# Kernel optimization log

Hardware: AMD Instinct MI355X
Metric: run time of the kernel (lower is better)

The kernel has to match this reference:

```python
import jax, jax.numpy as jnp
import numpy as np

BN_EPS = 1e-5

def _bn(x, gamma, beta, relu=True):
    # training-mode BatchNorm over all dims except channel (last)
    axes = tuple(range(x.ndim - 1))
    mu = jnp.mean(x, axes, keepdims=True)
    var = jnp.var(x, axes, keepdims=True)
    y = (x - mu) / jnp.sqrt(var + BN_EPS) * gamma + beta
    return jax.nn.relu(y) if relu else y

def _l2norm(x, eps):
    # F.normalize: x / max(||x||, eps)
    n = jnp.sqrt(jnp.sum(x * x, axis=-1, keepdims=True))
    return x / jnp.maximum(n, eps)

def setup_inputs() -> dict:
    key = jax.random.key(0)
    ks = jax.random.split(key, 16)
    B, N, H, W, C = 2, 512, 16, 32, 64
    IN_DIM = 10 + C + C + 2  # 140
    MLP3 = [128, 64]
    s = 0.02
    inp = {
        "warped_xyz": jax.random.normal(ks[0], (B, N, 3), jnp.float32),
        "warped_points": jax.random.normal(ks[1], (B, N, C), jnp.float32),
        "RF3": jax.random.normal(ks[2], (B, C, H, W), jnp.float32),
        "RF3_index": jax.random.normal(ks[3], (B, 3, H, W), jnp.float32),
        "lidar_z": jax.random.uniform(ks[4], (B, N, 1), jnp.float32),
        # conv1x1 stack (mlp3)
        "W1": jax.random.normal(ks[5], (IN_DIM, MLP3[0]), jnp.float32) * s,
        "b1": jnp.zeros((MLP3[0],), jnp.float32),
        "g1": jnp.ones((MLP3[0],), jnp.float32),
        "be1": jnp.zeros((MLP3[0],), jnp.float32),
        "W2": jax.random.normal(ks[6], (MLP3[0], MLP3[1]), jnp.float32) * s,
        "b2": jnp.zeros((MLP3[1],), jnp.float32),
        "g2": jnp.ones((MLP3[1],), jnp.float32),
        "be2": jnp.zeros((MLP3[1],), jnp.float32),
        # conv1d stack (mlp4 = [feats_dim//2], then 2 logits)
        "M1w": jax.random.normal(ks[7], (MLP3[1], MLP3[1] // 2), jnp.float32) * s,
        "M1b": jnp.zeros((MLP3[1] // 2,), jnp.float32),
        "M1g": jnp.ones((MLP3[1] // 2,), jnp.float32),
        "M1be": jnp.zeros((MLP3[1] // 2,), jnp.float32),
        "M2w": jax.random.normal(ks[8], (MLP3[1] // 2, 2), jnp.float32) * s,
        "M2b": jnp.zeros((2,), jnp.float32),
    }
    return inp

def reference(warped_xyz, warped_points, RF3, RF3_index, lidar_z,
              W1, b1, g1, be1, W2, b2, g2, be2,
              M1w, M1b, M1g, M1be, M2w, M2b):
    B, N, _ = warped_xyz.shape
    _, Ci, H, W_ = RF3.shape
    M = H * W_
    RF3_bnc = RF3.transpose(0, 2, 3, 1).reshape(B, M, Ci)          # [B,M,C]
    idx_bnc = RF3_index.transpose(0, 2, 3, 1).reshape(B, M, 3)     # [B,M,3]

    src_xyz = warped_xyz[:, :, None, :]                             # [B,N,1,3]
    dst_xyz = idx_bnc[:, None, :, :]                                # [B,1,M,3]
    euc = (src_xyz - dst_xyz)[..., :2]                              # [B,N,M,2]
    euc_norm = jnp.sqrt(euc[..., 0:1] ** 2 + euc[..., 1:2] ** 2)    # [B,N,M,1]

    xyz_z = (warped_xyz * lidar_z)[:, :, None, :]                   # [B,N,1,3]
    src_pts = warped_points[:, :, None, :]                          # [B,N,1,C]
    dst_pts = RF3_bnc[:, None, :, :]                                # [B,1,M,C]

    geom = jnp.concatenate([
        jnp.broadcast_to(xyz_z, (B, N, M, 3)),
        jnp.broadcast_to(src_pts[..., :2], (B, N, M, 2)),
        jnp.broadcast_to(dst_xyz[..., :2], (B, N, M, 2)),
        euc, euc_norm], axis=-1)                                    # [B,N,M,10]
    desc = jnp.concatenate([
        jnp.broadcast_to(src_pts, (B, N, M, Ci)),
        jnp.broadcast_to(dst_pts, (B, N, M, Ci))], axis=-1)         # [B,N,M,2C]

    # cal_sim: cosine sim between lidar feats (src) and image feats (dst)
    src_n = _l2norm(warped_points, 1e-12)
    dst_n = _l2norm(RF3_bnc, 1e-12)
    cos = jnp.einsum('bnc,bmc->bnm', src_n, dst_n)                  # [B,N,M]
    s1 = cos / (jnp.max(cos, axis=2, keepdims=True) + 1e-6)         # src->dst norm
    s2 = cos / (jnp.max(cos, axis=1, keepdims=True) + 1e-10)        # dst->src norm
    sim = jnp.stack([s1, s2], axis=-1)                              # [B,N,M,2]

    feats = jnp.concatenate([geom, desc, sim], axis=-1)             # [B,N,M,140]
    feats = _bn(jnp.einsum('bnmi,io->bnmo', feats, W1) + b1, g1, be1)
    feats = _bn(jnp.einsum('bnmi,io->bnmo', feats, W2) + b2, g2, be2)

    aw = jax.nn.softmax(jnp.max(feats, axis=-1), axis=-1)           # [B,N,M]
    att = jnp.einsum('bnm,bnmc->bnc', aw, feats)                    # [B,N,C]

    att = _bn(att @ M1w + M1b, M1g, M1be)
    logits = att @ M2w + M2b                                        # [B,N,2]
    return logits
```

## Files before the change

kernel.cpp:

```cpp
#include <hip/hip_runtime.h>
#include <hip/hip_bf16.h>

#define B_ 2
#define N_ 512
#define M_ 512
#define C_ 64
#define O1 128
#define O2 64
#define O3 32
#define PBIG 524288.0f
#define P3   1024.0f

typedef short s8v __attribute__((ext_vector_type(8)));
typedef float f4v __attribute__((ext_vector_type(4)));

#define WS_SRCN 0
#define WS_DSTN 65536
#define WS_P0   0
#define WS_U    131072
#define WS_V    262144
#define WS_DXY  393216
#define WS_COS  395264
#define WS_RMAX 919552
#define WS_CMAX 920576
#define WS_ST1  921600
#define WS_ST2  925696
#define WS_ST3  927744
#define WS_Z    928768
#define WS_W2F  928768
#define WS_W9S  932864
#define WS_X2   961536

__device__ __forceinline__ unsigned fenc(float f){
  unsigned b = __float_as_uint(f);
  return (b & 0x80000000u) ? ~b : (b | 0x80000000u);
}
__device__ __forceinline__ float fdec(unsigned u){
  unsigned b = (u & 0x80000000u) ? (u & 0x7fffffffu) : ~u;
  return __uint_as_float(b);
}
__device__ __forceinline__ unsigned short f2bf(float f){
  unsigned u = __float_as_uint(f);
  unsigned r = (u + 0x7fffu + ((u >> 16) & 1u)) >> 16;
  return (unsigned short)r;
}
__device__ __forceinline__ float bf2f(unsigned short h){
  return __uint_as_float(((unsigned)h) << 16);
}
__device__ __forceinline__ unsigned pk_trunc(float lo, float hi){
  return __builtin_amdgcn_perm(__float_as_uint(hi), __float_as_uint(lo), 0x07060302u);
}
__device__ __forceinline__ f4v relu4(f4v z){
  z[0] = fmaxf(z[0], 0.f); z[1] = fmaxf(z[1], 0.f);
  z[2] = fmaxf(z[2], 0.f); z[3] = fmaxf(z[3], 0.f);
  return z;
}

__global__ __launch_bounds__(128) void k1a(const float* __restrict__ wxyz,
    const float* __restrict__ wpts, const float* __restrict__ lz,
    const float* __restrict__ W1, float* __restrict__ ws){
  int blk = blockIdx.x; int b = blk >> 9, n = blk & 511; int t = threadIdx.x;
  int bn = b*N_ + n;
  __shared__ float wp[64]; __shared__ float sxyz[3]; __shared__ float slz; __shared__ float srn;
  if (t < 64) wp[t] = wpts[bn*64 + t];
  if (t >= 64 && t < 67) sxyz[t-64] = wxyz[bn*3 + (t-64)];
  if (t == 67) slz = lz[bn];
  __syncthreads();
  if (t < 64){
    float v = wp[t]*wp[t];
    v += __shfl_down(v,32); v += __shfl_down(v,16); v += __shfl_down(v,8);
    v += __shfl_down(v,4);  v += __shfl_down(v,2);  v += __shfl_down(v,1);
    if (t == 0) srn = 1.0f / fmaxf(sqrtf(v), 1e-12f);
  }
  __syncthreads();
  if (t < 64) ws[WS_SRCN + bn*64 + t] = wp[t]*srn;
  int o = t;
  float x = sxyz[0], y = sxyz[1], z = sxyz[2], l = slz;
  float acc = x*l*W1[0*O1+o] + y*l*W1[1*O1+o] + z*l*W1[2*O1+o]
            + wp[0]*W1[3*O1+o] + wp[1]*W1[4*O1+o]
            + x*W1[7*O1+o] + y*W1[8*O1+o];
  #pragma unroll 8
  for (int c = 0; c < 64; ++c) acc += wp[c]*W1[(10+c)*O1+o];
  ws[WS_U + bn*O1 + o] = acc;
}

__global__ __launch_bounds__(128) void k1b(const float* __restrict__ rf3,
    const float* __restrict__ rf3i, const float* __restrict__ W1, float* __restrict__ ws){
  int blk = blockIdx.x; int b = blk >> 9, m = blk & 511; int t = threadIdx.x;
  int bm = b*M_ + m;
  __shared__ float rf[64]; __shared__ float sdx, sdy, srn;
  if (t < 64) rf[t] = rf3[(b*64 + t)*512 + m];
  if (t == 64) sdx = rf3i[(b*3 + 0)*512 + m];
  if (t == 65) sdy = rf3i[(b*3 + 1)*512 + m];
  __syncthreads();
  if (t < 64){
    float v = rf[t]*rf[t];
    v += __shfl_down(v,32); v += __shfl_down(v,16); v += __shfl_down(v,8);
    v += __shfl_down(v,4);  v += __shfl_down(v,2);  v += __shfl_down(v,1);
    if (t == 0) srn = 1.0f / fmaxf(sqrtf(v), 1e-12f);
  }
  __syncthreads();
  if (t < 64) ws[WS_DSTN + bm*64 + t] = rf[t]*srn;
  if (t == 0){ ws[WS_DXY + bm*2+0] = sdx; ws[WS_DXY + bm*2+1] = sdy; }
  int o = t;
  float acc = sdx*(W1[5*O1+o] - W1[7*O1+o]) + sdy*(W1[6*O1+o] - W1[8*O1+o]);
  #pragma unroll 8
  for (int c = 0; c < 64; ++c) acc += rf[c]*W1[(74+c)*O1+o];
  ws[WS_V + bm*O1 + o] = acc;
}

__global__ __launch_bounds__(256) void k2(float* __restrict__ ws){
  int blk = blockIdx.x; int b = blk >> 9, n = blk & 511; int t = threadIdx.x;
  int bn = b*N_ + n;
  __shared__ __align__(16) float sn[64];
  __shared__ float dnt[64*65];
  __shared__ float part[4*64];
  if (t < 64) sn[t] = ws[WS_SRCN + bn*64 + t];
  unsigned* cmax = (unsigned*)ws + WS_CMAX;
  float lmax = -1e30f;
  for (int chunk = 0; chunk < 8; ++chunk){
    __syncthreads();
    const float4* src = (const float4*)(ws + WS_DSTN + (size_t)(b*M_ + chunk*64)*64);
    #pragma unroll
    for (int i = 0; i < 4; ++i){
      float4 v = src[t + i*256];
      int base = (t + i*256)*4; int mm = base >> 6, c = base & 63;
      float* dp = &dnt[mm*65 + c];
      dp[0]=v.x; dp[1]=v.y; dp[2]=v.z; dp[3]=v.w;
    }
    __syncthreads();
    {
      int mm = t & 63, cg = t >> 6;
      const float* dr = &dnt[mm*65 + cg*16];
      const float* sr = &sn[cg*16];
      float p = 0.f;
      #pragma unroll
      for (int k = 0; k < 16; ++k) p += sr[k]*dr[k];
      part[cg*64 + mm] = p;
    }
    __syncthreads();
    if (t < 64){
      float d = part[t] + part[64+t] + part[128+t] + part[192+t];
      int m = chunk*64 + t;
      ws[WS_COS + bn*M_ + m] = d;
      atomicMax(&cmax[b*M_ + m], fenc(d));
      lmax = fmaxf(lmax, d);
    }
  }
  if (t < 64){
    lmax = fmaxf(lmax, __shfl_xor(lmax,32)); lmax = fmaxf(lmax, __shfl_xor(lmax,16));
    lmax = fmaxf(lmax, __shfl_xor(lmax,8));  lmax = fmaxf(lmax, __shfl_xor(lmax,4));
    lmax = fmaxf(lmax, __shfl_xor(lmax,2));  lmax = fmaxf(lmax, __shfl_xor(lmax,1));
    if (t == 0) ws[WS_RMAX + bn] = lmax;
  }
}

__global__ __launch_bounds__(256) void k3(const float* __restrict__ wxyz,
    const float* __restrict__ W1, const float* __restrict__ b1, float* __restrict__ ws){
  int blk = blockIdx.x; int b = blk >> 9, n = blk & 511; int t = threadIdx.x;
  int bn = b*N_ + n;
  __shared__ float s_en[512], s_s1[512], s_s2[512];
  __shared__ float sx, sy, srm;
  if (t == 0){ sx = wxyz[bn*3+0]; sy = wxyz[bn*3+1]; srm = ws[WS_RMAX+bn]; }
  __syncthreads();
  const unsigned* cmax = (const unsigned*)ws + WS_CMAX;
  #pragma unroll
  for (int i = 0; i < 2; ++i){
    int m = t + i*256;
    float dx = ws[WS_DXY + (b*M_+m)*2+0], dy = ws[WS_DXY + (b*M_+m)*2+1];
    float ex = sx-dx, ey = sy-dy;
    s_en[m] = sqrtf(ex*ex + ey*ey);
    float cv = ws[WS_COS + bn*M_ + m];
    s_s1[m] = cv/(srm + 1e-6f);
    s_s2[m] = cv/(fdec(cmax[b*M_+m]) + 1e-10f);
  }
  __syncthreads();
  int o = t & 127, mh = t >> 7;
  float u  = ws[WS_U + bn*O1 + o] + b1[o];
  float w9 = W1[9*O1+o], wa = W1[138*O1+o], wb = W1[139*O1+o];
  float sum = 0.f, ssq = 0.f;
  const float* Vp = ws + WS_V + b*M_*O1 + o;
  int mBeg = mh*256, mEnd = mBeg + 256;
  #pragma unroll 8
  for (int m = mBeg; m < mEnd; ++m){
    float xv = u + Vp[m*O1] + s_en[m]*w9 + s_s1[m]*wa + s_s2[m]*wb;
    sum += xv; ssq += xv*xv;
  }
  int rep = blk & 15;
  atomicAdd(&ws[WS_ST1 + rep*256 + o], sum);
  atomicAdd(&ws[WS_ST1 + rep*256 + 128 + o], ssq);
}

__global__ __launch_bounds__(128) void k3b(const float* __restrict__ W1,
    const float* __restrict__ b1, const float* __restrict__ g1,
    const float* __restrict__ be1, const float* __restrict__ W2, float* __restrict__ ws){
  int blk = blockIdx.x; int t = threadIdx.x;
  int o = t;
  float s = 0.f, q = 0.f;
  #pragma unroll
  for (int r = 0; r < 16; ++r){ s += ws[WS_ST1 + r*256 + o]; q += ws[WS_ST1 + r*256 + 128 + o]; }
  float mu = s/PBIG, var = q/PBIG - mu*mu;
  float istd = rsqrtf(var + 1e-5f);
  float A1 = g1[o]*istd, C1 = be1[o] - mu*A1;
  if (blk < 1024){
    int bn = blk;
    ws[WS_P0 + bn*O1 + o] = (ws[WS_U + bn*O1 + o] + b1[o])*A1 + C1;
  } else if (blk < 1040){
    int r0 = (blk - 1024)*64;
    for (int r = 0; r < 64; ++r)
      ws[WS_V + (size_t)(r0 + r)*O1 + o] *= A1;
  } else {
    ws[WS_W9S + o]       = W1[9*O1+o]*A1;
    ws[WS_W9S + 128 + o] = W1[138*O1+o]*A1;
    ws[WS_W9S + 256 + o] = W1[139*O1+o]*A1;
    unsigned short* wf = (unsigned short*)(ws + WS_W2F);
    for (int i = t; i < 8192; i += 128){
      int j = i & 7, ll = (i >> 3) & 63, ct = (i >> 9) & 3, k0q = i >> 11;
      int oo = k0q*32 + (ll >> 4)*8 + j, c = ct*16 + (ll & 15);
      wf[i] = f2bf(W2[oo*O2 + c]);
    }
  }
}

__global__ __launch_bounds__(256, 4) void k4(const float* __restrict__ wxyz,
    float* __restrict__ ws){
  int blk = blockIdx.x;
  int b = blk >> 11; int rem = blk & 2047; int n = rem >> 2; int mc = rem & 3;
  int t = threadIdx.x; int bn = b*N_ + n; int m0 = mc*128;
  __shared__ __align__(16) unsigned short wBf[8192];
  __shared__ __align__(16) float p0s[128], w9s[128], was[128], wbs[128];
  __shared__ float s_en[128], s_s1[128], s_s2[128];
  __shared__ float ls[64], lq[64];
  __shared__ float sx, sy, srm;
  if (t == 0){ sx = wxyz[bn*3+0]; sy = wxyz[bn*3+1]; srm = ws[WS_RMAX+bn]; }
  if (t < 64){ ls[t] = 0.f; lq[t] = 0.f; }
  {
    const s8v* g = (const s8v*)(ws + WS_W2F);
    s8v* l = (s8v*)wBf;
    #pragma unroll
    for (int c2 = 0; c2 < 4; ++c2) l[c2*256 + t] = g[c2*256 + t];
  }
  if (t < 128){
    p0s[t] = ws[WS_P0 + bn*O1 + t];
    w9s[t] = ws[WS_W9S + t];
    was[t] = ws[WS_W9S + 128 + t];
    wbs[t] = ws[WS_W9S + 256 + t];
  }
  __syncthreads();
  if (t < 128){
    int m = m0 + t;
    float dx = ws[WS_DXY + (b*M_+m)*2+0], dy = ws[WS_DXY + (b*M_+m)*2+1];
    float ex = sx-dx, ey = sy-dy;
    s_en[t] = sqrtf(ex*ex + ey*ey);
    float cv = ws[WS_COS + bn*M_ + m];
    s_s1[t] = cv/(srm + 1e-6f);
    s_s2[t] = cv/(fdec(((const unsigned*)ws)[WS_CMAX + b*M_+m]) + 1e-10f);
  }
  __syncthreads();
  int ll = t & 63, w = t >> 6, l16 = ll & 15, quad = ll >> 4;
  int mb = m0 + w*32;
  float en0 = s_en[w*32 + l16],     s10 = s_s1[w*32 + l16],     s20 = s_s2[w*32 + l16];
  float en1 = s_en[w*32 + 16 + l16], s11 = s_s1[w*32 + 16 + l16], s21 = s_s2[w*32 + 16 + l16];
  f4v acc[2][4];
  #pragma unroll
  for (int i = 0; i < 2; ++i)
    #pragma unroll
    for (int j = 0; j < 4; ++j) acc[i][j] = (f4v){0.f,0.f,0.f,0.f};
  const float* Vb = ws + WS_V + (size_t)(b*M_ + mb)*O1;
  union U8 { s8v v; unsigned u[4]; };
  #pragma unroll
  for (int k0q = 0; k0q < 4; ++k0q){
    int ko = k0q*32 + quad*8;
    f4v p0a = *(const f4v*)&p0s[ko], p0b = *(const f4v*)&p0s[ko+4];
    f4v w9a = *(const f4v*)&w9s[ko], w9b = *(const f4v*)&w9s[ko+4];
    f4v waa = *(const f4v*)&was[ko], wab = *(const f4v*)&was[ko+4];
    f4v wba = *(const f4v*)&wbs[ko], wbb = *(const f4v*)&wbs[ko+4];
    s8v af[2];
    #pragma unroll
    for (int mt = 0; mt < 2; ++mt){
      const float* vp = Vb + (size_t)(mt*16 + l16)*O1 + ko;
      f4v va = *(const f4v*)vp, vb = *(const f4v*)(vp+4);
      float en = mt ? en1 : en0, s1 = mt ? s11 : s10, s2 = mt ? s21 : s20;
      f4v za = relu4(p0a + va + en*w9a + s1*waa + s2*wba);
      f4v zb = relu4(p0b + vb + en*w9b + s1*wab + s2*wbb);
      U8 u8;
      u8.u[0] = pk_trunc(za[0], za[1]);
      u8.u[1] = pk_trunc(za[2], za[3]);
      u8.u[2] = pk_trunc(zb[0], zb[1]);
      u8.u[3] = pk_trunc(zb[2], zb[3]);
      af[mt] = u8.v;
    }
    #pragma unroll
    for (int ct = 0; ct < 4; ++ct){
      s8v bb = *(const s8v*)&wBf[((k0q*4 + ct)*64 + ll)*8];
      acc[0][ct] = __builtin_amdgcn_mfma_f32_16x16x32_bf16(bb, af[0], acc[0][ct], 0,0,0);
      acc[1][ct] = __builtin_amdgcn_mfma_f32_16x16x32_bf16(bb, af[1], acc[1][ct], 0,0,0);
    }
  }
  unsigned short* x2p = (unsigned short*)(ws + WS_X2) + (size_t)bn*M_*O2;
  #pragma unroll
  for (int ct = 0; ct < 4; ++ct){
    int c0 = ct*16 + quad*4;
    #pragma unroll
    for (int mt = 0; mt < 2; ++mt){
      int m = mb + mt*16 + l16;
      uint2 uv;
      uv.x = (unsigned)f2bf(acc[mt][ct][0]) | ((unsigned)f2bf(acc[mt][ct][1]) << 16);
      uv.y = (unsigned)f2bf(acc[mt][ct][2]) | ((unsigned)f2bf(acc[mt][ct][3]) << 16);
      *(uint2*)(x2p + (size_t)m*O2 + c0) = uv;
    }
    #pragma unroll
    for (int r = 0; r < 4; ++r){
      float s = acc[0][ct][r] + acc[1][ct][r];
      float q = acc[0][ct][r]*acc[0][ct][r] + acc[1][ct][r]*acc[1][ct][r];
      s += __shfl_xor(s,1); s += __shfl_xor(s,2); s += __shfl_xor(s,4); s += __shfl_xor(s,8);
      q += __shfl_xor(q,1); q += __shfl_xor(q,2); q += __shfl_xor(q,4); q += __shfl_xor(q,8);
      if (l16 == 0){ atomicAdd(&ls[c0 + r], s); atomicAdd(&lq[c0 + r], q); }
    }
  }
  __syncthreads();
  int rep = blk & 15;
  if (t < 64) atomicAdd(&ws[WS_ST2 + rep*128 + t], ls[t]);
  else if (t < 128) atomicAdd(&ws[WS_ST2 + rep*128 + t], lq[t-64]);
}

__global__ __launch_bounds__(256) void k5(const float* __restrict__ g2,
    const float* __restrict__ be2, const float* __restrict__ M1w,
    const float* __restrict__ M1b, float* __restrict__ ws){
  int blk = blockIdx.x; int b = blk >> 9, n = blk & 511; int t = threadIdx.x;
  int bn = b*N_ + n;
  __shared__ float sa2[64], sc2[64];
  __shared__ float s_mx[512];
  __shared__ float s_aw[512];
  __shared__ float red[256];
  __shared__ float part[32*64];
  __shared__ float s_att[64];
  __shared__ float sgmax, sinvS;
  if (t < 64){
    float s = 0.f, q = 0.f;
    #pragma unroll
    for (int r = 0; r < 16; ++r){ s += ws[WS_ST2 + r*128 + t]; q += ws[WS_ST2 + r*128 + 64 + t]; }
    float mu = s/PBIG, var = q/PBIG - mu*mu;
    float istd = rsqrtf(var + 1e-5f);
    float A2 = g2[t]*istd;
    sa2[t] = A2; sc2[t] = be2[t] - mu*A2;
  }
  __syncthreads();
  int j8 = t & 7, r32 = t >> 3;
  int c0 = j8*8;
  float a2r[8], c2r[8];
  #pragma unroll
  for (int j = 0; j < 8; ++j){ a2r[j] = sa2[c0+j]; c2r[j] = sc2[c0+j]; }
  const unsigned short* xp = (const unsigned short*)(ws + WS_X2) + (size_t)bn*M_*O2;
  s8v xv[16];
  #pragma unroll
  for (int s = 0; s < 16; ++s)
    xv[s] = *(const s8v*)(xp + (size_t)(s*32 + r32)*64 + c0);
  #pragma unroll
  for (int s = 0; s < 16; ++s){
    float mx = 0.f;
    #pragma unroll
    for (int j = 0; j < 8; ++j){
      float x = bf2f((unsigned short)xv[s][j]);
      float y = fmaxf(a2r[j]*x + c2r[j], 0.f);
      mx = fmaxf(mx, y);
    }
    mx = fmaxf(mx, __shfl_xor(mx,1));
    mx = fmaxf(mx, __shfl_xor(mx,2));
    mx = fmaxf(mx, __shfl_xor(mx,4));
    if (j8 == 0) s_mx[s*32 + r32] = mx;
  }
  __syncthreads();
  red[t] = fmaxf(s_mx[t], s_mx[t+256]);
  __syncthreads();
  for (int s = 128; s > 0; s >>= 1){ if (t < s) red[t] = fmaxf(red[t], red[t+s]); __syncthreads(); }
  if (t == 0) sgmax = red[0];
  __syncthreads();
  float e0 = expf(s_mx[t] - sgmax), e1 = expf(s_mx[t+256] - sgmax);
  s_aw[t] = e0; s_aw[t+256] = e1;
  red[t] = e0 + e1;
  __syncthreads();
  for (int s = 128; s > 0; s >>= 1){ if (t < s) red[t] += red[t+s]; __syncthreads(); }
  if (t == 0) sinvS = 1.0f / red[0];
  __syncthreads();
  float acc[8];
  #pragma unroll
  for (int j = 0; j < 8; ++j) acc[j] = 0.f;
  #pragma unroll
  for (int s = 0; s < 16; ++s){
    float aw = s_aw[s*32 + r32];
    #pragma unroll
    for (int j = 0; j < 8; ++j){
      float x = bf2f((unsigned short)xv[s][j]);
      float y = fmaxf(a2r[j]*x + c2r[j], 0.f);
      acc[j] += aw*y;
    }
  }
  #pragma unroll
  for (int j = 0; j < 8; ++j) part[r32*64 + c0 + j] = acc[j];
  __syncthreads();
  if (t < 64){
    float a = 0.f;
    #pragma unroll 8
    for (int r = 0; r < 32; ++r) a += part[r*64 + t];
    s_att[t] = a * sinvS;
  }
  __syncthreads();
  if (t < 32){
    float z = M1b[t];
    #pragma unroll 8
    for (int c = 0; c < 64; ++c) z += s_att[c]*M1w[c*32 + t];
    ws[WS_Z + bn*32 + t] = z;
    int rep = blk & 15;
    atomicAdd(&ws[WS_ST3 + rep*64 + t], z);
    atomicAdd(&ws[WS_ST3 + rep*64 + 32 + t], z*z);
  }
}

__global__ __launch_bounds__(256) void k6(const float* __restrict__ M1g,
    const float* __restrict__ M1be, const float* __restrict__ M2w,
    const float* __restrict__ M2b, const float* __restrict__ ws, float* __restrict__ out){
  int t = threadIdx.x; int s = blockIdx.x*256 + t;
  __shared__ float sa3[32], sc3[32];
  if (t < 32){
    float su = 0.f, q = 0.f;
    #pragma unroll
    for (int r = 0; r < 16; ++r){ su += ws[WS_ST3 + r*64 + t]; q += ws[WS_ST3 + r*64 + 32 + t]; }
    float mu = su/P3, var = q/P3 - mu*mu;
    float istd = rsqrtf(var + 1e-5f);
    float A3 = M1g[t]*istd;
    sa3[t] = A3; sc3[t] = M1be[t] - mu*A3;
  }
  __syncthreads();
  float a0 = M2b[0], a1 = M2b[1];
  #pragma unroll
  for (int j = 0; j < 32; ++j){
    float y = fmaxf(ws[WS_Z + s*32 + j]*sa3[j] + sc3[j], 0.f);
    a0 += y*M2w[j*2+0]; a1 += y*M2w[j*2+1];
  }
  out[s*2+0] = a0; out[s*2+1] = a1;
}

extern "C" void kernel_launch(void* const* d_in, const int* in_sizes, int n_in,
                              void* d_out, int out_size, void* d_ws, size_t ws_size,
                              hipStream_t stream){
  const float* wxyz = (const float*)d_in[0];
  const float* wpts = (const float*)d_in[1];
  const float* rf3  = (const float*)d_in[2];
  const float* rf3i = (const float*)d_in[3];
  const float* lz   = (const float*)d_in[4];
  const float* W1   = (const float*)d_in[5];
  const float* b1   = (const float*)d_in[6];
  const float* g1   = (const float*)d_in[7];
  const float* be1  = (const float*)d_in[8];
  const float* W2   = (const float*)d_in[9];
  const float* g2   = (const float*)d_in[11];
  const float* be2  = (const float*)d_in[12];
  const float* M1w  = (const float*)d_in[13];
  const float* M1b  = (const float*)d_in[14];
  const float* M1g  = (const float*)d_in[15];
  const float* M1be = (const float*)d_in[16];
  const float* M2w  = (const float*)d_in[17];
  const float* M2b  = (const float*)d_in[18];
  float* ws  = (float*)d_ws;
  float* out = (float*)d_out;
  hipMemsetAsync(ws + WS_CMAX, 0, (1024 + 4096 + 2048 + 1024)*sizeof(float), stream);
  k1a<<<1024,128,0,stream>>>(wxyz, wpts, lz, W1, ws);
  k1b<<<1024,128,0,stream>>>(rf3, rf3i, W1, ws);
  k2 <<<1024,256,0,stream>>>(ws);
  k3 <<<1024,256,0,stream>>>(wxyz, W1, b1, ws);
  k3b<<<1041,128,0,stream>>>(W1, b1, g1, be1, W2, ws);
  k4 <<<4096,256,0,stream>>>(wxyz, ws);
  k5 <<<1024,256,0,stream>>>(g2, be2, M1w, M1b, ws);
  k6 <<<4,256,0,stream>>>(M1g, M1be, M2w, M2b, ws, out);
}
```

Baseline: 239.3 us.

## Merge k1 kernels, replace atomic max with reduction kernel, widen stat replicas

```diff
diff --git a/kernel.cpp b/kernel.cpp
--- a/kernel.cpp
+++ b/kernel.cpp
@@ -18,27 +18,19 @@
 #define WS_DSTN 65536
 #define WS_P0   0
 #define WS_U    131072
+#define WS_Z    131072
 #define WS_V    262144
 #define WS_DXY  393216
 #define WS_COS  395264
 #define WS_RMAX 919552
-#define WS_CMAX 920576
-#define WS_ST1  921600
-#define WS_ST2  925696
-#define WS_ST3  927744
-#define WS_Z    928768
-#define WS_W2F  928768
-#define WS_W9S  932864
+#define WS_ST1  920576
+#define WS_ST2  936960
+#define WS_ST3  945152
+#define WS_CMAX 949248
+#define WS_W2F  950272
+#define WS_W9S  954368
 #define WS_X2   961536
 
-__device__ __forceinline__ unsigned fenc(float f){
-  unsigned b = __float_as_uint(f);
-  return (b & 0x80000000u) ? ~b : (b | 0x80000000u);
-}
-__device__ __forceinline__ float fdec(unsigned u){
-  unsigned b = (u & 0x80000000u) ? (u & 0x7fffffffu) : ~u;
-  return __uint_as_float(b);
-}
 __device__ __forceinline__ unsigned short f2bf(float f){
   unsigned u = __float_as_uint(f);
   unsigned r = (u + 0x7fffu + ((u >> 16) & 1u)) >> 16;
@@ -56,57 +48,58 @@
   return z;
 }
 
-__global__ __launch_bounds__(128) void k1a(const float* __restrict__ wxyz,
+__global__ __launch_bounds__(128) void k1(const float* __restrict__ wxyz,
     const float* __restrict__ wpts, const float* __restrict__ lz,
+    const float* __restrict__ rf3, const float* __restrict__ rf3i,
     const float* __restrict__ W1, float* __restrict__ ws){
-  int blk = blockIdx.x; int b = blk >> 9, n = blk & 511; int t = threadIdx.x;
-  int bn = b*N_ + n;
-  __shared__ float wp[64]; __shared__ float sxyz[3]; __shared__ float slz; __shared__ float srn;
-  if (t < 64) wp[t] = wpts[bn*64 + t];
-  if (t >= 64 && t < 67) sxyz[t-64] = wxyz[bn*3 + (t-64)];
-  if (t == 67) slz = lz[bn];
-  __syncthreads();
-  if (t < 64){
-    float v = wp[t]*wp[t];
-    v += __shfl_down(v,32); v += __shfl_down(v,16); v += __shfl_down(v,8);
-    v += __shfl_down(v,4);  v += __shfl_down(v,2);  v += __shfl_down(v,1);
-    if (t == 0) srn = 1.0f / fmaxf(sqrtf(v), 1e-12f);
-  }
-  __syncthreads();
-  if (t < 64) ws[WS_SRCN + bn*64 + t] = wp[t]*srn;
-  int o = t;
-  float x = sxyz[0], y = sxyz[1], z = sxyz[2], l = slz;
-  float acc = x*l*W1[0*O1+o] + y*l*W1[1*O1+o] + z*l*W1[2*O1+o]
-            + wp[0]*W1[3*O1+o] + wp[1]*W1[4*O1+o]
-            + x*W1[7*O1+o] + y*W1[8*O1+o];
-  #pragma unroll 8
-  for (int c = 0; c < 64; ++c) acc += wp[c]*W1[(10+c)*O1+o];
-  ws[WS_U + bn*O1 + o] = acc;
-}
-
-__global__ __launch_bounds__(128) void k1b(const float* __restrict__ rf3,
-    const float* __restrict__ rf3i, const float* __restrict__ W1, float* __restrict__ ws){
-  int blk = blockIdx.x; int b = blk >> 9, m = blk & 511; int t = threadIdx.x;
-  int bm = b*M_ + m;
-  __shared__ float rf[64]; __shared__ float sdx, sdy, srn;
-  if (t < 64) rf[t] = rf3[(b*64 + t)*512 + m];
-  if (t == 64) sdx = rf3i[(b*3 + 0)*512 + m];
-  if (t == 65) sdy = rf3i[(b*3 + 1)*512 + m];
-  __syncthreads();
-  if (t < 64){
-    float v = rf[t]*rf[t];
-    v += __shfl_down(v,32); v += __shfl_down(v,16); v += __shfl_down(v,8);
-    v += __shfl_down(v,4);  v += __shfl_down(v,2);  v += __shfl_down(v,1);
-    if (t == 0) srn = 1.0f / fmaxf(sqrtf(v), 1e-12f);
-  }
-  __syncthreads();
-  if (t < 64) ws[WS_DSTN + bm*64 + t] = rf[t]*srn;
-  if (t == 0){ ws[WS_DXY + bm*2+0] = sdx; ws[WS_DXY + bm*2+1] = sdy; }
-  int o = t;
-  float acc = sdx*(W1[5*O1+o] - W1[7*O1+o]) + sdy*(W1[6*O1+o] - W1[8*O1+o]);
-  #pragma unroll 8
-  for (int c = 0; c < 64; ++c) acc += rf[c]*W1[(74+c)*O1+o];
-  ws[WS_V + bm*O1 + o] = acc;
+  int t = threadIdx.x;
+  if (blockIdx.x < 1024){
+    int blk = blockIdx.x; int b = blk >> 9, n = blk & 511;
+    int bn = b*N_ + n;
+    __shared__ float wp[64]; __shared__ float sxyz[3]; __shared__ float slz; __shared__ float srn;
+    if (t < 64) wp[t] = wpts[bn*64 + t];
+    if (t >= 64 && t < 67) sxyz[t-64] = wxyz[bn*3 + (t-64)];
+    if (t == 67) slz = lz[bn];
+    __syncthreads();
+    if (t < 64){
+      float v = wp[t]*wp[t];
+      v += __shfl_down(v,32); v += __shfl_down(v,16); v += __shfl_down(v,8);
+      v += __shfl_down(v,4);  v += __shfl_down(v,2);  v += __shfl_down(v,1);
+      if (t == 0) srn = 1.0f / fmaxf(sqrtf(v), 1e-12f);
+    }
+    __syncthreads();
+    if (t < 64) ws[WS_SRCN + bn*64 + t] = wp[t]*srn;
+    int o = t;
+    float x = sxyz[0], y = sxyz[1], z = sxyz[2], l = slz;
+    float acc = x*l*W1[0*O1+o] + y*l*W1[1*O1+o] + z*l*W1[2*O1+o]
+              + wp[0]*W1[3*O1+o] + wp[1]*W1[4*O1+o]
+              + x*W1[7*O1+o] + y*W1[8*O1+o];
+    #pragma unroll 8
+    for (int c = 0; c < 64; ++c) acc += wp[c]*W1[(10+c)*O1+o];
+    ws[WS_U + bn*O1 + o] = acc;
+  } else {
+    int blk = blockIdx.x - 1024; int b = blk >> 9, m = blk & 511;
+    int bm = b*M_ + m;
+    __shared__ float rf[64]; __shared__ float sdx, sdy, srn2;
+    if (t < 64) rf[t] = rf3[(b*64 + t)*512 + m];
+    if (t == 64) sdx = rf3i[(b*3 + 0)*512 + m];
+    if (t == 65) sdy = rf3i[(b*3 + 1)*512 + m];
+    __syncthreads();
+    if (t < 64){
+      float v = rf[t]*rf[t];
+      v += __shfl_down(v,32); v += __shfl_down(v,16); v += __shfl_down(v,8);
+      v += __shfl_down(v,4);  v += __shfl_down(v,2);  v += __shfl_down(v,1);
+      if (t == 0) srn2 = 1.0f / fmaxf(sqrtf(v), 1e-12f);
+    }
+    __syncthreads();
+    if (t < 64) ws[WS_DSTN + bm*64 + t] = rf[t]*srn2;
+    if (t == 0){ ws[WS_DXY + bm*2+0] = sdx; ws[WS_DXY + bm*2+1] = sdy; }
+    int o = t;
+    float acc = sdx*(W1[5*O1+o] - W1[7*O1+o]) + sdy*(W1[6*O1+o] - W1[8*O1+o]);
+    #pragma unroll 8
+    for (int c = 0; c < 64; ++c) acc += rf[c]*W1[(74+c)*O1+o];
+    ws[WS_V + bm*O1 + o] = acc;
+  }
 }
 
 __global__ __launch_bounds__(256) void k2(float* __restrict__ ws){
@@ -116,8 +109,6 @@
   __shared__ float dnt[64*65];
   __shared__ float part[4*64];
   if (t < 64) sn[t] = ws[WS_SRCN + bn*64 + t];
-  unsigned* cmax = (unsigned*)ws + WS_CMAX;
-  float lmax = -1e30f;
   for (int chunk = 0; chunk < 8; ++chunk){
     __syncthreads();
     const float4* src = (const float4*)(ws + WS_DSTN + (size_t)(b*M_ + chunk*64)*64);
@@ -141,54 +132,81 @@
     __syncthreads();
     if (t < 64){
       float d = part[t] + part[64+t] + part[128+t] + part[192+t];
-      int m = chunk*64 + t;
-      ws[WS_COS + bn*M_ + m] = d;
-      atomicMax(&cmax[b*M_ + m], fenc(d));
-      lmax = fmaxf(lmax, d);
-    }
-  }
-  if (t < 64){
-    lmax = fmaxf(lmax, __shfl_xor(lmax,32)); lmax = fmaxf(lmax, __shfl_xor(lmax,16));
-    lmax = fmaxf(lmax, __shfl_xor(lmax,8));  lmax = fmaxf(lmax, __shfl_xor(lmax,4));
-    lmax = fmaxf(lmax, __shfl_xor(lmax,2));  lmax = fmaxf(lmax, __shfl_xor(lmax,1));
-    if (t == 0) ws[WS_RMAX + bn] = lmax;
+      ws[WS_COS + bn*M_ + chunk*64 + t] = d;
+    }
+  }
+}
+
+__global__ __launch_bounds__(256) void k2r(float* __restrict__ ws){
+  int blk = blockIdx.x; int t = threadIdx.x;
+  if (blk < 4){
+    int b = blk >> 1, nh = blk & 1;
+    int bn = b*N_ + nh*256 + t;
+    const float4* rp = (const float4*)(ws + WS_COS + (size_t)bn*M_);
+    float mx = -3.4e38f;
+    #pragma unroll 8
+    for (int i = 0; i < 128; ++i){
+      float4 v = rp[i];
+      mx = fmaxf(mx, fmaxf(fmaxf(v.x, v.y), fmaxf(v.z, v.w)));
+    }
+    ws[WS_RMAX + bn] = 1.0f / (mx + 1e-6f);
+  } else {
+    __shared__ float sred[256];
+    int q = blk - 4; int b = q >> 2; int mcol = (q & 3)*128 + (t & 127);
+    int nh = t >> 7;
+    float mx = -3.4e38f;
+    for (int i = 0; i < 256; ++i){
+      int n = nh*256 + i;
+      mx = fmaxf(mx, ws[WS_COS + (size_t)(b*N_ + n)*M_ + mcol]);
+    }
+    sred[t] = mx;
+    __syncthreads();
+    if (t < 128){
+      float m2 = fmaxf(sred[t], sred[t+128]);
+      ws[WS_CMAX + b*M_ + mcol] = 1.0f / (m2 + 1e-10f);
+    }
   }
 }
 
 __global__ __launch_bounds__(256) void k3(const float* __restrict__ wxyz,
     const float* __restrict__ W1, const float* __restrict__ b1, float* __restrict__ ws){
-  int blk = blockIdx.x; int b = blk >> 9, n = blk & 511; int t = threadIdx.x;
-  int bn = b*N_ + n;
-  __shared__ float s_en[512], s_s1[512], s_s2[512];
-  __shared__ float sx, sy, srm;
-  if (t == 0){ sx = wxyz[bn*3+0]; sy = wxyz[bn*3+1]; srm = ws[WS_RMAX+bn]; }
-  __syncthreads();
-  const unsigned* cmax = (const unsigned*)ws + WS_CMAX;
-  #pragma unroll
-  for (int i = 0; i < 2; ++i){
-    int m = t + i*256;
-    float dx = ws[WS_DXY + (b*M_+m)*2+0], dy = ws[WS_DXY + (b*M_+m)*2+1];
-    float ex = sx-dx, ey = sy-dy;
-    s_en[m] = sqrtf(ex*ex + ey*ey);
-    float cv = ws[WS_COS + bn*M_ + m];
-    s_s1[m] = cv/(srm + 1e-6f);
-    s_s2[m] = cv/(fdec(cmax[b*M_+m]) + 1e-10f);
+  int blk = blockIdx.x; int bn = blk >> 1, half = blk & 1; int t = threadIdx.x;
+  int b = bn >> 9; int mbase = half*256;
+  __shared__ float s_en[256], s_s1[256], s_s2[256];
+  __shared__ float sred[512];
+  float sx = wxyz[bn*3+0], sy = wxyz[bn*3+1];
+  float ri = ws[WS_RMAX + bn];
+  {
+    int m = mbase + t;
+    float2 d = *(const float2*)(ws + WS_DXY + (size_t)(b*M_+m)*2);
+    float ex = sx-d.x, ey = sy-d.y;
+    s_en[t] = sqrtf(ex*ex + ey*ey);
+    float cv = ws[WS_COS + (size_t)bn*M_ + m];
+    s_s1[t] = cv*ri;
+    s_s2[t] = cv*ws[WS_CMAX + b*M_ + m];
   }
   __syncthreads();
   int o = t & 127, mh = t >> 7;
   float u  = ws[WS_U + bn*O1 + o] + b1[o];
   float w9 = W1[9*O1+o], wa = W1[138*O1+o], wb = W1[139*O1+o];
   float sum = 0.f, ssq = 0.f;
-  const float* Vp = ws + WS_V + b*M_*O1 + o;
-  int mBeg = mh*256, mEnd = mBeg + 256;
+  const float* Vp = ws + WS_V + (size_t)b*M_*O1 + o;
+  int lBeg = mh*128, lEnd = lBeg + 128;
   #pragma unroll 8
-  for (int m = mBeg; m < mEnd; ++m){
-    float xv = u + Vp[m*O1] + s_en[m]*w9 + s_s1[m]*wa + s_s2[m]*wb;
+  for (int ml = lBeg; ml < lEnd; ++ml){
+    float xv = u + Vp[(size_t)(mbase+ml)*O1] + s_en[ml]*w9 + s_s1[ml]*wa + s_s2[ml]*wb;
     sum += xv; ssq += xv*xv;
   }
-  int rep = blk & 15;
-  atomicAdd(&ws[WS_ST1 + rep*256 + o], sum);
-  atomicAdd(&ws[WS_ST1 + rep*256 + 128 + o], ssq);
+  sred[mh*128 + o] = sum;
+  sred[256 + mh*128 + o] = ssq;
+  __syncthreads();
+  if (t < 128){
+    float S = sred[t] + sred[128+t];
+    float Q = sred[256+t] + sred[384+t];
+    int rep = blk & 63;
+    atomicAdd(&ws[WS_ST1 + rep*256 + t], S);
+    atomicAdd(&ws[WS_ST1 + rep*256 + 128 + t], Q);
+  }
 }
 
 __global__ __launch_bounds__(128) void k3b(const float* __restrict__ W1,
@@ -197,8 +215,8 @@
   int blk = blockIdx.x; int t = threadIdx.x;
   int o = t;
   float s = 0.f, q = 0.f;
-  #pragma unroll
-  for (int r = 0; r < 16; ++r){ s += ws[WS_ST1 + r*256 + o]; q += ws[WS_ST1 + r*256 + 128 + o]; }
+  #pragma unroll 8
+  for (int r = 0; r < 64; ++r){ s += ws[WS_ST1 + r*256 + o]; q += ws[WS_ST1 + r*256 + 128 + o]; }
   float mu = s/PBIG, var = q/PBIG - mu*mu;
   float istd = rsqrtf(var + 1e-5f);
   float A1 = g1[o]*istd, C1 = be1[o] - mu*A1;
@@ -229,17 +247,14 @@
   int t = threadIdx.x; int bn = b*N_ + n; int m0 = mc*128;
   __shared__ __align__(16) unsigned short wBf[8192];
   __shared__ __align__(16) float p0s[128], w9s[128], was[128], wbs[128];
-  __shared__ float s_en[128], s_s1[128], s_s2[128];
   __shared__ float ls[64], lq[64];
-  __shared__ float sx, sy, srm;
-  if (t == 0){ sx = wxyz[bn*3+0]; sy = wxyz[bn*3+1]; srm = ws[WS_RMAX+bn]; }
-  if (t < 64){ ls[t] = 0.f; lq[t] = 0.f; }
   {
     const s8v* g = (const s8v*)(ws + WS_W2F);
     s8v* l = (s8v*)wBf;
     #pragma unroll
     for (int c2 = 0; c2 < 4; ++c2) l[c2*256 + t] = g[c2*256 + t];
   }
+  if (t < 64){ ls[t] = 0.f; lq[t] = 0.f; }
   if (t < 128){
     p0s[t] = ws[WS_P0 + bn*O1 + t];
     w9s[t] = ws[WS_W9S + t];
@@ -247,54 +262,60 @@
     wbs[t] = ws[WS_W9S + 256 + t];
   }
   __syncthreads();
-  if (t < 128){
-    int m = m0 + t;
-    float dx = ws[WS_DXY + (b*M_+m)*2+0], dy = ws[WS_DXY + (b*M_+m)*2+1];
-    float ex = sx-dx, ey = sy-dy;
-    s_en[t] = sqrtf(ex*ex + ey*ey);
-    float cv = ws[WS_COS + bn*M_ + m];
-    s_s1[t] = cv/(srm + 1e-6f);
-    s_s2[t] = cv/(fdec(((const unsigned*)ws)[WS_CMAX + b*M_+m]) + 1e-10f);
-  }
-  __syncthreads();
   int ll = t & 63, w = t >> 6, l16 = ll & 15, quad = ll >> 4;
   int mb = m0 + w*32;
-  float en0 = s_en[w*32 + l16],     s10 = s_s1[w*32 + l16],     s20 = s_s2[w*32 + l16];
-  float en1 = s_en[w*32 + 16 + l16], s11 = s_s1[w*32 + 16 + l16], s21 = s_s2[w*32 + 16 + l16];
+  int mA = mb + l16, mB = mb + 16 + l16;
+  float sx = wxyz[bn*3+0], sy = wxyz[bn*3+1];
+  float ri = ws[WS_RMAX + bn];
+  float2 dA = *(const float2*)(ws + WS_DXY + (size_t)(b*M_+mA)*2);
+  float2 dB = *(const float2*)(ws + WS_DXY + (size_t)(b*M_+mB)*2);
+  float cvA = ws[WS_COS + (size_t)bn*M_ + mA], cvB = ws[WS_COS + (size_t)bn*M_ + mB];
+  float ciA = ws[WS_CMAX + b*M_ + mA],         ciB = ws[WS_CMAX + b*M_ + mB];
+  float exA = sx-dA.x, eyA = sy-dA.y; float en0 = sqrtf(exA*exA + eyA*eyA);
+  float exB = sx-dB.x, eyB = sy-dB.y; float en1 = sqrtf(exB*exB + eyB*eyB);
+  float s10 = cvA*ri, s20 = cvA*ciA;
+  float s11 = cvB*ri, s21 = cvB*ciB;
+  const float* vpA = ws + WS_V + (size_t)(b*M_+mA)*O1;
+  const float* vpB = ws + WS_V + (size_t)(b*M_+mB)*O1;
   f4v acc[2][4];
   #pragma unroll
   for (int i = 0; i < 2; ++i)
     #pragma unroll
     for (int j = 0; j < 4; ++j) acc[i][j] = (f4v){0.f,0.f,0.f,0.f};
-  const float* Vb = ws + WS_V + (size_t)(b*M_ + mb)*O1;
   union U8 { s8v v; unsigned u[4]; };
+  f4v bufA[2][2], bufB[2][2];
+  {
+    int k0 = quad*8;
+    bufA[0][0] = *(const f4v*)(vpA + k0); bufA[0][1] = *(const f4v*)(vpA + k0 + 4);
+    bufB[0][0] = *(const f4v*)(vpB + k0); bufB[0][1] = *(const f4v*)(vpB + k0 + 4);
+  }
   #pragma unroll
   for (int k0q = 0; k0q < 4; ++k0q){
+    int pc = k0q & 1, pn = pc ^ 1;
+    if (k0q < 3){
+      int kn = (k0q+1)*32 + quad*8;
+      bufA[pn][0] = *(const f4v*)(vpA + kn); bufA[pn][1] = *(const f4v*)(vpA + kn + 4);
+      bufB[pn][0] = *(const f4v*)(vpB + kn); bufB[pn][1] = *(const f4v*)(vpB + kn + 4);
+    }
     int ko = k0q*32 + quad*8;
     f4v p0a = *(const f4v*)&p0s[ko], p0b = *(const f4v*)&p0s[ko+4];
     f4v w9a = *(const f4v*)&w9s[ko], w9b = *(const f4v*)&w9s[ko+4];
     f4v waa = *(const f4v*)&was[ko], wab = *(const f4v*)&was[ko+4];
     f4v wba = *(const f4v*)&wbs[ko], wbb = *(const f4v*)&wbs[ko+4];
-    s8v af[2];
-    #pragma unroll
-    for (int mt = 0; mt < 2; ++mt){
-      const float* vp = Vb + (size_t)(mt*16 + l16)*O1 + ko;
-      f4v va = *(const f4v*)vp, vb = *(const f4v*)(vp+4);
-      float en = mt ? en1 : en0, s1 = mt ? s11 : s10, s2 = mt ? s21 : s20;
-      f4v za = relu4(p0a + va + en*w9a + s1*waa + s2*wba);
-      f4v zb = relu4(p0b + vb + en*w9b + s1*wab + s2*wbb);
-      U8 u8;
-      u8.u[0] = pk_trunc(za[0], za[1]);
-      u8.u[1] = pk_trunc(za[2], za[3]);
-      u8.u[2] = pk_trunc(zb[0], zb[1]);
-      u8.u[3] = pk_trunc(zb[2], zb[3]);
-      af[mt] = u8.v;
-    }
+    f4v zaA = relu4(p0a + bufA[pc][0] + en0*w9a + s10*waa + s20*wba);
+    f4v zbA = relu4(p0b + bufA[pc][1] + en0*w9b + s10*wab + s20*wbb);
+    f4v zaB = relu4(p0a + bufB[pc][0] + en1*w9a + s11*waa + s21*wba);
+    f4v zbB = relu4(p0b + bufB[pc][1] + en1*w9b + s11*wab + s21*wbb);
+    U8 uA, uB;
+    uA.u[0] = pk_trunc(zaA[0], zaA[1]); uA.u[1] = pk_trunc(zaA[2], zaA[3]);
+    uA.u[2] = pk_trunc(zbA[0], zbA[1]); uA.u[3] = pk_trunc(zbA[2], zbA[3]);
+    uB.u[0] = pk_trunc(zaB[0], zaB[1]); uB.u[1] = pk_trunc(zaB[2], zaB[3]);
+    uB.u[2] = pk_trunc(zbB[0], zbB[1]); uB.u[3] = pk_trunc(zbB[2], zbB[3]);
     #pragma unroll
     for (int ct = 0; ct < 4; ++ct){
       s8v bb = *(const s8v*)&wBf[((k0q*4 + ct)*64 + ll)*8];
-      acc[0][ct] = __builtin_amdgcn_mfma_f32_16x16x32_bf16(bb, af[0], acc[0][ct], 0,0,0);
-      acc[1][ct] = __builtin_amdgcn_mfma_f32_16x16x32_bf16(bb, af[1], acc[1][ct], 0,0,0);
+      acc[0][ct] = __builtin_amdgcn_mfma_f32_16x16x32_bf16(bb, uA.v, acc[0][ct], 0,0,0);
+      acc[1][ct] = __builtin_amdgcn_mfma_f32_16x16x32_bf16(bb, uB.v, acc[1][ct], 0,0,0);
     }
   }
   unsigned short* x2p = (unsigned short*)(ws + WS_X2) + (size_t)bn*M_*O2;
@@ -319,7 +340,7 @@
     }
   }
   __syncthreads();
-  int rep = blk & 15;
+  int rep = blk & 63;
   if (t < 64) atomicAdd(&ws[WS_ST2 + rep*128 + t], ls[t]);
   else if (t < 128) atomicAdd(&ws[WS_ST2 + rep*128 + t], lq[t-64]);
 }
@@ -338,8 +359,8 @@
   __shared__ float sgmax, sinvS;
   if (t < 64){
     float s = 0.f, q = 0.f;
-    #pragma unroll
-    for (int r = 0; r < 16; ++r){ s += ws[WS_ST2 + r*128 + t]; q += ws[WS_ST2 + r*128 + 64 + t]; }
+    #pragma unroll 8
+    for (int r = 0; r < 64; ++r){ s += ws[WS_ST2 + r*128 + t]; q += ws[WS_ST2 + r*128 + 64 + t]; }
     float mu = s/PBIG, var = q/PBIG - mu*mu;
     float istd = rsqrtf(var + 1e-5f);
     float A2 = g2[t]*istd;
@@ -411,7 +432,7 @@
     #pragma unroll 8
     for (int c = 0; c < 64; ++c) z += s_att[c]*M1w[c*32 + t];
     ws[WS_Z + bn*32 + t] = z;
-    int rep = blk & 15;
+    int rep = blk & 63;
     atomicAdd(&ws[WS_ST3 + rep*64 + t], z);
     atomicAdd(&ws[WS_ST3 + rep*64 + 32 + t], z*z);
   }
@@ -424,8 +445,8 @@
   __shared__ float sa3[32], sc3[32];
   if (t < 32){
     float su = 0.f, q = 0.f;
-    #pragma unroll
-    for (int r = 0; r < 16; ++r){ su += ws[WS_ST3 + r*64 + t]; q += ws[WS_ST3 + r*64 + 32 + t]; }
+    #pragma unroll 8
+    for (int r = 0; r < 64; ++r){ su += ws[WS_ST3 + r*64 + t]; q += ws[WS_ST3 + r*64 + 32 + t]; }
     float mu = su/P3, var = q/P3 - mu*mu;
     float istd = rsqrtf(var + 1e-5f);
     float A3 = M1g[t]*istd;
@@ -464,11 +485,11 @@
   const float* M2b  = (const float*)d_in[18];
   float* ws  = (float*)d_ws;
   float* out = (float*)d_out;
-  hipMemsetAsync(ws + WS_CMAX, 0, (1024 + 4096 + 2048 + 1024)*sizeof(float), stream);
-  k1a<<<1024,128,0,stream>>>(wxyz, wpts, lz, W1, ws);
-  k1b<<<1024,128,0,stream>>>(rf3, rf3i, W1, ws);
+  hipMemsetAsync(ws + WS_ST1, 0, 28672*sizeof(float), stream);
+  k1 <<<2048,128,0,stream>>>(wxyz, wpts, lz, rf3, rf3i, W1, ws);
   k2 <<<1024,256,0,stream>>>(ws);
-  k3 <<<1024,256,0,stream>>>(wxyz, W1, b1, ws);
+  k2r<<<12,256,0,stream>>>(ws);
+  k3 <<<2048,256,0,stream>>>(wxyz, W1, b1, ws);
   k3b<<<1041,128,0,stream>>>(W1, b1, g1, be1, W2, ws);
   k4 <<<4096,256,0,stream>>>(wxyz, ws);
   k5 <<<1024,256,0,stream>>>(g2, be2, M1w, M1b, ws);
```

After: 274.3 us. +14.6%, slower.
